# Performance work log

Hardware: AMD Instinct MI355X
Metric: run time of the kernel (lower is better)

## Reference

```python
import jax, jax.numpy as jnp
import numpy as np

HEADS = 4
ALPHA = 0.2
NEG = -9.0e15


def _layer(h, adj_mask, W, linW, linb, qkvW, qkvb, a, concat):
    # One GraphSelfAttentionLayer (eval mode: dropout off).
    F_out = W.shape[-1]
    n = h.shape[0]
    Wh = (h @ W) @ linW + linb                      # [N, F]
    qkv = Wh @ qkvW + qkvb                          # [N, 3F]
    q, k, v = jnp.split(qkv, 3, axis=-1)
    to_heads = lambda t: t.reshape(n, HEADS, F_out // HEADS).transpose(1, 0, 2)
    q, k, v = to_heads(q), to_heads(k), to_heads(v)  # [H, N, d]
    # note: scale uses out_features (not per-head d), matching the source
    dots = jax.nn.softmax(jnp.einsum('hid,hjd->hij', q, k) * (F_out ** -0.5), axis=-1)
    Wh0 = jnp.einsum('hij,hjd->hid', dots, v).transpose(1, 0, 2).reshape(n, F_out)
    Wh0 = jax.nn.softmax(Wh0, axis=-1)
    # decomposed all-pairs GAT score: e[i,j] = leakyrelu(Wh_i.a1 + Wh_j.a2)
    f1 = Wh @ a[:F_out]                             # [N]
    f2 = Wh @ a[F_out:]
    e = jax.nn.leaky_relu(f1[:, None] + f2[None, :], ALPHA)
    logits = jnp.where(adj_mask, e + dots.sum(0), NEG)
    att = jax.nn.softmax(logits, axis=1)
    hp = att @ Wh + Wh0
    return jax.nn.elu(hp) if concat else hp


def setup_inputs() -> dict:
    key = jax.random.key(0)
    ks = jax.random.split(key, 16)
    N, NFEAT, NHID, NOUT, H = 3072, 128, 32, 64, 4
    s = 0.1
    return {
        'x': jax.random.normal(ks[0], (N, NFEAT), jnp.float32),
        'adj': jax.random.randint(ks[1], (N, N), 0, 2, dtype=jnp.int32),
        'W_h': jax.random.normal(ks[2], (H, NFEAT, NHID), jnp.float32) * s,
        'lin_W_h': jax.random.normal(ks[3], (H, NHID, NHID), jnp.float32) * s,
        'lin_b_h': jax.random.normal(ks[4], (H, NHID), jnp.float32) * s,
        'qkv_W_h': jax.random.normal(ks[5], (H, NHID, 3 * NHID), jnp.float32) * s,
        'qkv_b_h': jax.random.normal(ks[6], (H, 3 * NHID), jnp.float32) * s,
        'a_h': jax.random.normal(ks[7], (H, 2 * NHID), jnp.float32) * s,
        'W_o': jax.random.normal(ks[8], (NHID * H, NOUT), jnp.float32) * s,
        'lin_W_o': jax.random.normal(ks[9], (NOUT, NOUT), jnp.float32) * s,
        'lin_b_o': jax.random.normal(ks[10], (NOUT,), jnp.float32) * s,
        'qkv_W_o': jax.random.normal(ks[11], (NOUT, 3 * NOUT), jnp.float32) * s,
        'qkv_b_o': jax.random.normal(ks[12], (3 * NOUT,), jnp.float32) * s,
        'a_o': jax.random.normal(ks[13], (2 * NOUT,), jnp.float32) * s,
    }


def reference(x, adj, W_h, lin_W_h, lin_b_h, qkv_W_h, qkv_b_h, a_h,
              W_o, lin_W_o, lin_b_o, qkv_W_o, qkv_b_o, a_o):
    mask = adj > 0
    heads_out = jax.vmap(
        lambda W, lW, lb, qW, qb, a: _layer(x, mask, W, lW, lb, qW, qb, a, True)
    )(W_h, lin_W_h, lin_b_h, qkv_W_h, qkv_b_h, a_h)      # [H, N, NHID]
    n = x.shape[0]
    x1 = jax.nn.elu(heads_out.transpose(1, 0, 2).reshape(n, -1))  # cat(dim=1) then elu
    out = jax.nn.elu(_layer(x1, mask, W_o, lin_W_o, lin_b_o, qkv_W_o, qkv_b_o, a_o, False))
    return out
```

## Files before the change

### kernel.cpp

```cpp
#include <hip/hip_runtime.h>
#include <hip/hip_bf16.h>

#define LOG2E 1.4426950408889634f
#define LOG2LOG2E 0.5287663729448977f

typedef unsigned int u32;
typedef float f32x16 __attribute__((ext_vector_type(16)));
typedef short sh8 __attribute__((ext_vector_type(8)));

union FR { u32 u[4]; sh8 s; };

__device__ __forceinline__ u32 cvt_pk_bf16(float lo, float hi){
  u32 r;
  asm volatile("v_cvt_pk_bf16_f32 %0, %1, %2" : "=v"(r) : "v"(lo), "v"(hi));
  return r;
}

__device__ __forceinline__ float asum16(const float* s){
  float a0=s[0]+s[8],  a1=s[1]+s[9],  a2=s[2]+s[10], a3=s[3]+s[11];
  float a4=s[4]+s[12], a5=s[5]+s[13], a6=s[6]+s[14], a7=s[7]+s[15];
  a0+=a4; a1+=a5; a2+=a6; a3+=a7;
  a0+=a2; a1+=a3;
  return a0+a1;
}

template<int W>
__device__ __forceinline__ float wred_max(float v){
  #pragma unroll
  for (int o=1;o<W;o<<=1) v = fmaxf(v, __shfl_xor(v,o));
  return v;
}
template<int W>
__device__ __forceinline__ float wred_sum(float v){
  #pragma unroll
  for (int o=1;o<W;o<<=1) v += __shfl_xor(v,o);
  return v;
}

__global__ __launch_bounds__(256) void k_mask(const int* __restrict__ adj, u32* __restrict__ mk){
  int id = blockIdx.x*256 + threadIdx.x;
  const int4* src = (const int4*)(adj + (size_t)id*32);
  u32 m = 0;
  #pragma unroll
  for (int g=0; g<8; g++){
    int4 v = src[g];
    if (v.x>0) m |= 1u<<(g*4+0);
    if (v.y>0) m |= 1u<<(g*4+1);
    if (v.z>0) m |= 1u<<(g*4+2);
    if (v.w>0) m |= 1u<<(g*4+3);
  }
  mk[id] = m;
}

template<int FIN, int F>
__global__ __launch_bounds__(256) void k_pre_a(const float* __restrict__ xg, const float* __restrict__ Wg,
    const float* __restrict__ lWg, const float* __restrict__ lbg, float* __restrict__ Whg, int N)
{
  const int h = blockIdx.y;
  const int row = blockIdx.x*256 + threadIdx.x;
  __shared__ float Wl[FIN*F];
  __shared__ float lWl[F*F];
  __shared__ float lbl[F];
  for (int i=threadIdx.x;i<FIN*F;i+=256) Wl[i]=Wg[(size_t)h*FIN*F+i];
  for (int i=threadIdx.x;i<F*F;i+=256) lWl[i]=lWg[(size_t)h*F*F+i];
  if (threadIdx.x<F) lbl[threadIdx.x]=lbg[h*F+threadIdx.x];
  __syncthreads();
  float t[F];
  #pragma unroll
  for (int c=0;c<F;c++) t[c]=0.f;
  const float4* xr = (const float4*)(xg + (size_t)row*FIN);
  for (int k4=0;k4<FIN/4;k4++){
    float4 xv = xr[k4];
    float xs[4]={xv.x,xv.y,xv.z,xv.w};
    #pragma unroll
    for (int kk=0;kk<4;kk++){
      float x1 = xs[kk];
      const float* wrow = Wl + (k4*4+kk)*F;
      #pragma unroll
      for (int c=0;c<F;c++) t[c] = fmaf(x1, wrow[c], t[c]);
    }
  }
  float wh[F];
  #pragma unroll
  for (int c=0;c<F;c++) wh[c]=lbl[c];
  #pragma unroll
  for (int k=0;k<F;k++){
    float tv=t[k];
    #pragma unroll
    for (int c=0;c<F;c++) wh[c]=fmaf(tv, lWl[k*F+c], wh[c]);
  }
  float4* dst=(float4*)(Whg + ((size_t)h*N+row)*F);
  #pragma unroll
  for (int c4=0;c4<F/4;c4++) dst[c4]=make_float4(wh[c4*4],wh[c4*4+1],wh[c4*4+2],wh[c4*4+3]);
}

template<int F, int GPR>
__global__ __launch_bounds__(256) void k_pre_b(const float* __restrict__ Whg, const float* __restrict__ qWg,
   const float* __restrict__ qbg, const float* __restrict__ ag,
   float* __restrict__ qg, float* __restrict__ kg, float* __restrict__ vg,
   float* __restrict__ f1g, float* __restrict__ f2g, int N)
{
  constexpr int ROWS = 256/GPR;
  constexpr int GC3  = 3*F/GPR;
  const int h = blockIdx.y;
  const int rl = threadIdx.x / GPR, grp = threadIdx.x % GPR;
  const int row = blockIdx.x*ROWS + rl;
  __shared__ float qWl[F*3*F];
  __shared__ float qbl[3*F];
  __shared__ float al[2*F];
  __shared__ float whl[ROWS][F+1];
  for (int i=threadIdx.x;i<F*3*F;i+=256) qWl[i]=qWg[(size_t)h*F*3*F+i];
  if (threadIdx.x<3*F) qbl[threadIdx.x]=qbg[h*3*F+threadIdx.x];
  if (threadIdx.x<2*F) al[threadIdx.x]=ag[h*2*F+threadIdx.x];
  {
    const float4* wsrc = (const float4*)(Whg + ((size_t)h*N+row)*F);
    #pragma unroll
    for (int c4=0;c4<2;c4++){
      float4 t = wsrc[grp*2+c4];
      int b = grp*8+c4*4;
      whl[rl][b]=t.x; whl[rl][b+1]=t.y; whl[rl][b+2]=t.z; whl[rl][b+3]=t.w;
    }
  }
  __syncthreads();
  float acc[GC3];
  #pragma unroll
  for (int c=0;c<GC3;c++) acc[c]=qbl[grp*GC3+c];
  for (int k=0;k<F;k++){
    float wv = whl[rl][k];
    #pragma unroll
    for (int c=0;c<GC3;c++) acc[c]=fmaf(wv, qWl[k*3*F + grp*GC3 + c], acc[c]);
  }
  size_t base = ((size_t)h*N+row)*F;
  #pragma unroll
  for (int c=0;c<GC3;c++){
    int col = grp*GC3+c;
    if (col < F)        qg[base+col]       = acc[c];
    else if (col < 2*F) kg[base+col-F]     = acc[c];
    else                vg[base+col-2*F]   = acc[c];
  }
  if (grp<2){
    const float* av = al + grp*F;
    float s=0.f;
    for (int k=0;k<F;k++) s = fmaf(whl[rl][k], av[k], s);
    (grp? f2g:f1g)[(size_t)h*N+row] = s;
  }
}

template<int S>
__global__ __launch_bounds__(256,4) void k_sweep1_mfma32(const float* __restrict__ qg, const float* __restrict__ kg,
    const float* __restrict__ vg, float* __restrict__ pml, float* __restrict__ pw, int N, float qscale)
{
  constexpr int F=32, LROW=33;
  const int h = blockIdx.z;
  const int sc = blockIdx.y;
  const int JC = N/S;
  const int wid = threadIdx.x>>6;
  const int lane = threadIdx.x&63;
  const int l31 = lane&31;
  const int half = lane>>5;
  const int itile = blockIdx.x*4 + wid;
  const int i = itile*32 + l31;
  __shared__ float vt[32*LROW];

  sh8 qf[4];
  {
    const float* qrow = qg + ((size_t)h*N + i)*F;
    #pragma unroll
    for (int hh=0;hh<4;hh++){
      FR u;
      #pragma unroll
      for (int p=0;p<4;p++){
        float lo = half? 0.f : qrow[hh*8+2*p]*qscale;
        float hi = half? 0.f : qrow[hh*8+2*p+1]*qscale;
        u.u[p] = cvt_pk_bf16(lo,hi);
      }
      qf[hh]=u.s;
    }
  }
  f32x16 C, Zv;
  #pragma unroll
  for (int r=0;r<16;r++){ C[r]=0.f; Zv[r]=0.f; }
  float l[4];
  #pragma unroll
  for (int hh=0;hh<4;hh++) l[hh]=0.f;
  const sh8 zf = {0,0,0,0,0,0,0,0};

  const int j0 = sc*JC;
  for (int jt=0; jt<JC; jt+=32){
    __syncthreads();
    {
      const float4* vs = (const float4*)(vg + ((size_t)h*N + j0+jt)*F);
      int idx = threadIdx.x;
      int j = idx>>3, c4 = idx&7;
      float4 b = vs[idx];
      float* vd = vt + j*LROW + c4*4;
      vd[0]=b.x; vd[1]=b.y; vd[2]=b.z; vd[3]=b.w;
    }
    __syncthreads();
    const float* krow = kg + ((size_t)h*N + j0+jt + l31)*F;
    sh8 vA[2];
    #pragma unroll
    for (int c=0;c<2;c++){
      FR u;
      #pragma unroll
      for (int p=0;p<4;p++){
        int jl = c*16 + half*8 + 2*p;
        u.u[p]=cvt_pk_bf16(vt[jl*LROW + l31], vt[(jl+1)*LROW + l31]);
      }
      vA[c]=u.s;
    }
    #pragma unroll
    for (int hh=0;hh<4;hh++){
      sh8 kf;
      {
        FR u;
        float4 ka = *(const float4*)(krow + hh*8);
        float4 kb = *(const float4*)(krow + hh*8 + 4);
        u.u[0]=cvt_pk_bf16(ka.x,ka.y);
        u.u[1]=cvt_pk_bf16(ka.z,ka.w);
        u.u[2]=cvt_pk_bf16(kb.x,kb.y);
        u.u[3]=cvt_pk_bf16(kb.z,kb.w);
        kf=u.s;
      }
      f32x16 Sacc = __builtin_amdgcn_mfma_f32_32x32x16_bf16(kf, qf[hh], Zv, 0,0,0);
      float p[16];
      #pragma unroll
      for (int r=0;r<16;r++) p[r] = exp2f(Sacc[r]);
      l[hh] += asum16(p);
      const bool own = ((l31>>3)==hh);
      #pragma unroll
      for (int c=0;c<2;c++){
        u32 a01 = cvt_pk_bf16(p[c*8+0], p[c*8+1]);
        u32 a23 = cvt_pk_bf16(p[c*8+2], p[c*8+3]);
        u32 b01 = cvt_pk_bf16(p[c*8+4], p[c*8+5]);
        u32 b23 = cvt_pk_bf16(p[c*8+6], p[c*8+7]);
        u32 a01s = __shfl_xor(a01,32);
        u32 a23s = __shfl_xor(a23,32);
        u32 b01s = __shfl_xor(b01,32);
        u32 b23s = __shfl_xor(b23,32);
        FR bf;
        bf.u[0] = half? b01s : a01;
        bf.u[1] = half? b23s : a23;
        bf.u[2] = half? b01  : a01s;
        bf.u[3] = half? b23  : a23s;
        sh8 av = own ? vA[c] : zf;
        C = __builtin_amdgcn_mfma_f32_32x32x16_bf16(av, bf.s, C, 0,0,0);
      }
    }
  }
  float lt[4];
  #pragma unroll
  for (int hh=0;hh<4;hh++) lt[hh] = l[hh] + __shfl_xor(l[hh],32);
  if (half==0){
    float* pb = pml + ((size_t)(h*S+sc)*8)*N + i;
    #pragma unroll
    for (int hh=0;hh<4;hh++){ pb[(size_t)hh*N]=0.f; pb[(size_t)(4+hh)*N]=lt[hh]; }
  }
  {
    float* pv = pw + ((size_t)(h*S+sc)*N + i)*F;
    #pragma unroll
    for (int hh=0;hh<4;hh++){
      *(float4*)(pv + 8*hh + 4*half) = make_float4(C[hh*4],C[hh*4+1],C[hh*4+2],C[hh*4+3]);
    }
  }
}

template<int S>
__global__ __launch_bounds__(256,4) void k_sweep2_mfma32(const float* __restrict__ qg, const float* __restrict__ kg,
    const float* __restrict__ whg, const float* __restrict__ f1g, const float* __restrict__ f2g,
    const float* __restrict__ mstar, const float* __restrict__ invl, const u32* __restrict__ mk,
    float* __restrict__ p2ml, float* __restrict__ php, int N, float qscale)
{
  constexpr int F=32, LROW=33;
  const int h = blockIdx.z;
  const int sc = blockIdx.y;
  const int JC = N/S;
  const int wid = threadIdx.x>>6;
  const int lane = threadIdx.x&63;
  const int l31 = lane&31;
  const int half = lane>>5;
  const int itile = blockIdx.x*4 + wid;
  const int i = itile*32 + l31;
  const int nw = N>>5;
  __shared__ float wt[32*LROW];
  __shared__ float f2s[32];

  sh8 qf[4];
  {
    const float* qrow = qg + ((size_t)h*N + i)*F;
    #pragma unroll
    for (int hh=0;hh<4;hh++){
      FR u;
      #pragma unroll
      for (int p=0;p<4;p++){
        float lo = half? 0.f : qrow[hh*8+2*p]*qscale;
        float hi = half? 0.f : qrow[hh*8+2*p+1]*qscale;
        u.u[p] = cvt_pk_bf16(lo,hi);
      }
      qf[hh]=u.s;
    }
  }
  float cc[4];
  #pragma unroll
  for (int hh=0;hh<4;hh++){
    float msv = mstar[((size_t)(h*4+hh))*N+i];
    float ilv = invl [((size_t)(h*4+hh))*N+i];
    cc[hh] = log2f(ilv) - msv + LOG2LOG2E;
  }
  const float f1 = f1g[(size_t)h*N+i];
  f32x16 C, Zv;
  #pragma unroll
  for (int r=0;r<16;r++){ C[r]=0.f; Zv[r]=0.f; }
  float L=0.f;

  const int j0 = sc*JC;
  for (int jt=0; jt<JC; jt+=32){
    __syncthreads();
    {
      const float4* ws = (const float4*)(whg + ((size_t)h*N + j0+jt)*F);
      int idx = threadIdx.x;
      int j = idx>>3, c4 = idx&7;
      float4 b = ws[idx];
      float* wd = wt + j*LROW + c4*4;
      wd[0]=b.x; wd[1]=b.y; wd[2]=b.z; wd[3]=b.w;
      if (threadIdx.x<32) f2s[threadIdx.x] = f2g[(size_t)h*N + j0+jt+threadIdx.x];
    }
    __syncthreads();
    const float* krow = kg + ((size_t)h*N + j0+jt + l31)*F;
    float ds[16];
    #pragma unroll
    for (int r=0;r<16;r++) ds[r]=0.f;
    #pragma unroll
    for (int hh=0;hh<4;hh++){
      sh8 kf;
      {
        FR u;
        float4 ka = *(const float4*)(krow + hh*8);
        float4 kb = *(const float4*)(krow + hh*8 + 4);
        u.u[0]=cvt_pk_bf16(ka.x,ka.y);
        u.u[1]=cvt_pk_bf16(ka.z,ka.w);
        u.u[2]=cvt_pk_bf16(kb.x,kb.y);
        u.u[3]=cvt_pk_bf16(kb.z,kb.w);
        kf=u.s;
      }
      f32x16 Sacc = __builtin_amdgcn_mfma_f32_32x32x16_bf16(kf, qf[hh], Zv, 0,0,0);
      float ch = cc[hh];
      #pragma unroll
      for (int r=0;r<16;r++) ds[r] += exp2f(Sacc[r] + ch);
    }
    u32 mw = mk[(size_t)i*nw + ((j0+jt)>>5)];
    float w[16];
    #pragma unroll
    for (int r=0;r<16;r++){
      int jo = (r&3)+8*(r>>2)+4*half;
      float e = f1 + f2s[jo];
      e = (e>=0.f)? e : 0.2f*e;
      float ev = exp2f(fmaf(e, LOG2E, ds[r]));
      w[r] = ((mw>>jo)&1u) ? ev : 0.f;
    }
    L += asum16(w);
    #pragma unroll
    for (int c=0;c<2;c++){
      sh8 whA;
      {
        FR u;
        #pragma unroll
        for (int p=0;p<4;p++){
          int jl = c*16 + half*8 + 2*p;
          u.u[p]=cvt_pk_bf16(wt[jl*LROW + l31], wt[(jl+1)*LROW + l31]);
        }
        whA=u.s;
      }
      u32 a01 = cvt_pk_bf16(w[c*8+0], w[c*8+1]);
      u32 a23 = cvt_pk_bf16(w[c*8+2], w[c*8+3]);
      u32 b01 = cvt_pk_bf16(w[c*8+4], w[c*8+5]);
      u32 b23 = cvt_pk_bf16(w[c*8+6], w[c*8+7]);
      u32 a01s = __shfl_xor(a01,32);
      u32 a23s = __shfl_xor(a23,32);
      u32 b01s = __shfl_xor(b01,32);
      u32 b23s = __shfl_xor(b23,32);
      FR bf;
      bf.u[0] = half? b01s : a01;
      bf.u[1] = half? b23s : a23;
      bf.u[2] = half? b01  : a01s;
      bf.u[3] = half? b23  : a23s;
      C = __builtin_amdgcn_mfma_f32_32x32x16_bf16(whA, bf.s, C, 0,0,0);
    }
  }
  L = L + __shfl_xor(L,32);
  if (half==0){
    float* pb = p2ml + ((size_t)(h*S+sc)*2)*N + i;
    pb[0]=0.f; pb[(size_t)N]=L;
  }
  {
    float* pv = php + ((size_t)(h*S+sc)*N + i)*F;
    #pragma unroll
    for (int g=0;g<4;g++)
      *(float4*)(pv + 8*g + 4*half) = make_float4(C[g*4],C[g*4+1],C[g*4+2],C[g*4+3]);
  }
}

template<int S>
__global__ __launch_bounds__(256,4) void k_sweep1_mfma64(const float* __restrict__ qg, const float* __restrict__ kg,
    const float* __restrict__ vg, float* __restrict__ pml, float* __restrict__ pw, int N, float qscale)
{
  constexpr int F=64, LROW=65;
  const int h = blockIdx.z;
  const int sc = blockIdx.y;
  const int JC = N/S;
  const int wid = threadIdx.x>>6;
  const int lane = threadIdx.x&63;
  const int l31 = lane&31;
  const int half = lane>>5;
  const int itile = blockIdx.x*4 + wid;
  const int i = itile*32 + l31;
  __shared__ float vt[32*LROW];

  sh8 qf[4];
  {
    const float* qrow = qg + ((size_t)h*N + i)*F;
    #pragma unroll
    for (int hh=0;hh<4;hh++){
      FR u;
      #pragma unroll
      for (int p=0;p<4;p++)
        u.u[p] = cvt_pk_bf16(qrow[hh*16 + 8*half + 2*p]*qscale, qrow[hh*16 + 8*half + 2*p+1]*qscale);
      qf[hh]=u.s;
    }
  }
  f32x16 C0, C1, Zv;
  #pragma unroll
  for (int r=0;r<16;r++){ C0[r]=0.f; C1[r]=0.f; Zv[r]=0.f; }
  float l[4];
  #pragma unroll
  for (int hh=0;hh<4;hh++) l[hh]=0.f;
  const sh8 zf = {0,0,0,0,0,0,0,0};

  const int j0 = sc*JC;
  for (int jt=0; jt<JC; jt+=32){
    __syncthreads();
    {
      const float4* vs = (const float4*)(vg + ((size_t)h*N + j0+jt)*F);
      #pragma unroll
      for (int q2=0;q2<2;q2++){
        int idx = q2*256 + threadIdx.x;
        int j = idx>>4, c4 = idx&15;
        float4 b = vs[idx];
        float* vd = vt + j*LROW + c4*4;
        vd[0]=b.x; vd[1]=b.y; vd[2]=b.z; vd[3]=b.w;
      }
    }
    __syncthreads();
    const float* krow = kg + ((size_t)h*N + j0+jt + l31)*F;
    sh8 vA[2][2];
    #pragma unroll
    for (int ch=0;ch<2;ch++)
      #pragma unroll
      for (int c=0;c<2;c++){
        FR u;
        #pragma unroll
        for (int p=0;p<4;p++){
          int jl = c*16 + half*8 + 2*p;
          u.u[p]=cvt_pk_bf16(vt[jl*LROW + ch*32 + l31], vt[(jl+1)*LROW + ch*32 + l31]);
        }
        vA[ch][c]=u.s;
      }
    #pragma unroll
    for (int hh=0;hh<4;hh++){
      sh8 kf;
      {
        FR u;
        float4 ka = *(const float4*)(krow + hh*16 + 8*half);
        float4 kb = *(const float4*)(krow + hh*16 + 8*half + 4);
        u.u[0]=cvt_pk_bf16(ka.x,ka.y);
        u.u[1]=cvt_pk_bf16(ka.z,ka.w);
        u.u[2]=cvt_pk_bf16(kb.x,kb.y);
        u.u[3]=cvt_pk_bf16(kb.z,kb.w);
        kf=u.s;
      }
      f32x16 Sacc = __builtin_amdgcn_mfma_f32_32x32x16_bf16(kf, qf[hh], Zv, 0,0,0);
      f32x16 &Cr = (hh>>1)? C1 : C0;
      float p[16];
      #pragma unroll
      for (int r=0;r<16;r++) p[r] = exp2f(Sacc[r]);
      l[hh] += asum16(p);
      const bool own = ((l31>>4) == (hh&1));
      #pragma unroll
      for (int c=0;c<2;c++){
        u32 a01 = cvt_pk_bf16(p[c*8+0], p[c*8+1]);
        u32 a23 = cvt_pk_bf16(p[c*8+2], p[c*8+3]);
        u32 b01 = cvt_pk_bf16(p[c*8+4], p[c*8+5]);
        u32 b23 = cvt_pk_bf16(p[c*8+6], p[c*8+7]);
        u32 a01s = __shfl_xor(a01,32);
        u32 a23s = __shfl_xor(a23,32);
        u32 b01s = __shfl_xor(b01,32);
        u32 b23s = __shfl_xor(b23,32);
        FR bf;
        bf.u[0] = half? b01s : a01;
        bf.u[1] = half? b23s : a23;
        bf.u[2] = half? b01  : a01s;
        bf.u[3] = half? b23  : a23s;
        sh8 av = own ? vA[hh>>1][c] : zf;
        Cr = __builtin_amdgcn_mfma_f32_32x32x16_bf16(av, bf.s, Cr, 0,0,0);
      }
    }
  }
  float lt[4];
  #pragma unroll
  for (int hh=0;hh<4;hh++) lt[hh] = l[hh] + __shfl_xor(l[hh],32);
  if (half==0){
    float* pb = pml + ((size_t)(h*S+sc)*8)*N + i;
    #pragma unroll
    for (int hh=0;hh<4;hh++){ pb[(size_t)hh*N]=0.f; pb[(size_t)(4+hh)*N]=lt[hh]; }
  }
  {
    float* pv = pw + ((size_t)(h*S+sc)*N + i)*F;
    #pragma unroll
    for (int g=0;g<4;g++){
      *(float4*)(pv + 8*g + 4*half)      = make_float4(C0[g*4],C0[g*4+1],C0[g*4+2],C0[g*4+3]);
      *(float4*)(pv + 32 + 8*g + 4*half) = make_float4(C1[g*4],C1[g*4+1],C1[g*4+2],C1[g*4+3]);
    }
  }
}

template<int S>
__global__ __launch_bounds__(256,4) void k_sweep2_mfma64(const float* __restrict__ qg, const float* __restrict__ kg,
    const float* __restrict__ whg, const float* __restrict__ f1g, const float* __restrict__ f2g,
    const float* __restrict__ mstar, const float* __restrict__ invl, const u32* __restrict__ mk,
    float* __restrict__ p2ml, float* __restrict__ php, int N, float qscale)
{
  constexpr int F=64, LROW=65;
  const int h = blockIdx.z;
  const int sc = blockIdx.y;
  const int JC = N/S;
  const int wid = threadIdx.x>>6;
  const int lane = threadIdx.x&63;
  const int l31 = lane&31;
  const int half = lane>>5;
  const int itile = blockIdx.x*4 + wid;
  const int i = itile*32 + l31;
  const int nw = N>>5;
  __shared__ float wt[32*LROW];
  __shared__ float f2s[32];

  sh8 qf[4];
  {
    const float* qrow = qg + ((size_t)h*N + i)*F;
    #pragma unroll
    for (int hh=0;hh<4;hh++){
      FR u;
      #pragma unroll
      for (int p=0;p<4;p++)
        u.u[p] = cvt_pk_bf16(qrow[hh*16 + 8*half + 2*p]*qscale, qrow[hh*16 + 8*half + 2*p+1]*qscale);
      qf[hh]=u.s;
    }
  }
  float cc[4];
  #pragma unroll
  for (int hh=0;hh<4;hh++){
    float msv = mstar[((size_t)(h*4+hh))*N+i];
    float ilv = invl [((size_t)(h*4+hh))*N+i];
    cc[hh] = log2f(ilv) - msv + LOG2LOG2E;
  }
  const float f1 = f1g[(size_t)h*N+i];
  f32x16 C0, C1, Zv;
  #pragma unroll
  for (int r=0;r<16;r++){ C0[r]=0.f; C1[r]=0.f; Zv[r]=0.f; }
  float L=0.f;

  const int j0 = sc*JC;
  for (int jt=0; jt<JC; jt+=32){
    __syncthreads();
    {
      const float4* ws = (const float4*)(whg + ((size_t)h*N + j0+jt)*F);
      #pragma unroll
      for (int q2=0;q2<2;q2++){
        int idx = q2*256 + threadIdx.x;
        int j = idx>>4, c4 = idx&15;
        float4 b = ws[idx];
        float* wd = wt + j*LROW + c4*4;
        wd[0]=b.x; wd[1]=b.y; wd[2]=b.z; wd[3]=b.w;
      }
      if (threadIdx.x<32) f2s[threadIdx.x] = f2g[(size_t)h*N + j0+jt+threadIdx.x];
    }
    __syncthreads();
    const float* krow = kg + ((size_t)h*N + j0+jt + l31)*F;
    float ds[16];
    #pragma unroll
    for (int r=0;r<16;r++) ds[r]=0.f;
    #pragma unroll
    for (int hh=0;hh<4;hh++){
      sh8 kf;
      {
        FR u;
        float4 ka = *(const float4*)(krow + hh*16 + 8*half);
        float4 kb = *(const float4*)(krow + hh*16 + 8*half + 4);
        u.u[0]=cvt_pk_bf16(ka.x,ka.y);
        u.u[1]=cvt_pk_bf16(ka.z,ka.w);
        u.u[2]=cvt_pk_bf16(kb.x,kb.y);
        u.u[3]=cvt_pk_bf16(kb.z,kb.w);
        kf=u.s;
      }
      f32x16 Sacc = __builtin_amdgcn_mfma_f32_32x32x16_bf16(kf, qf[hh], Zv, 0,0,0);
      float ch = cc[hh];
      #pragma unroll
      for (int r=0;r<16;r++) ds[r] += exp2f(Sacc[r] + ch);
    }
    u32 mw = mk[(size_t)i*nw + ((j0+jt)>>5)];
    float w[16];
    #pragma unroll
    for (int r=0;r<16;r++){
      int jo = (r&3)+8*(r>>2)+4*half;
      float e = f1 + f2s[jo];
      e = (e>=0.f)? e : 0.2f*e;
      float ev = exp2f(fmaf(e, LOG2E, ds[r]));
      w[r] = ((mw>>jo)&1u) ? ev : 0.f;
    }
    L += asum16(w);
    #pragma unroll
    for (int c=0;c<2;c++){
      u32 a01 = cvt_pk_bf16(w[c*8+0], w[c*8+1]);
      u32 a23 = cvt_pk_bf16(w[c*8+2], w[c*8+3]);
      u32 b01 = cvt_pk_bf16(w[c*8+4], w[c*8+5]);
      u32 b23 = cvt_pk_bf16(w[c*8+6], w[c*8+7]);
      u32 a01s = __shfl_xor(a01,32);
      u32 a23s = __shfl_xor(a23,32);
      u32 b01s = __shfl_xor(b01,32);
      u32 b23s = __shfl_xor(b23,32);
      FR bf;
      bf.u[0] = half? b01s : a01;
      bf.u[1] = half? b23s : a23;
      bf.u[2] = half? b01  : a01s;
      bf.u[3] = half? b23  : a23s;
      #pragma unroll
      for (int ch=0;ch<2;ch++){
        sh8 whA;
        {
          FR u;
          #pragma unroll
          for (int p=0;p<4;p++){
            int jl = c*16 + half*8 + 2*p;
            u.u[p]=cvt_pk_bf16(wt[jl*LROW + ch*32 + l31], wt[(jl+1)*LROW + ch*32 + l31]);
          }
          whA=u.s;
        }
        if (ch) C1 = __builtin_amdgcn_mfma_f32_32x32x16_bf16(whA, bf.s, C1, 0,0,0);
        else    C0 = __builtin_amdgcn_mfma_f32_32x32x16_bf16(whA, bf.s, C0, 0,0,0);
      }
    }
  }
  L = L + __shfl_xor(L,32);
  if (half==0){
    float* pb = p2ml + ((size_t)(h*S+sc)*2)*N + i;
    pb[0]=0.f; pb[(size_t)N]=L;
  }
  {
    float* pv = php + ((size_t)(h*S+sc)*N + i)*F;
    #pragma unroll
    for (int g=0;g<4;g++){
      *(float4*)(pv + 8*g + 4*half)      = make_float4(C0[g*4],C0[g*4+1],C0[g*4+2],C0[g*4+3]);
      *(float4*)(pv + 32 + 8*g + 4*half) = make_float4(C1[g*4],C1[g*4+1],C1[g*4+2],C1[g*4+3]);
    }
  }
}

template<int S>
__global__ __launch_bounds__(256) void k_stats1(const float* __restrict__ pml, float* __restrict__ wgt1,
    float* __restrict__ mstar, float* __restrict__ invl, int N)
{
  const int h = blockIdx.y>>2, hh = blockIdx.y&3;
  const int row = blockIdx.x*256 + threadIdx.x;
  float mv[S];
  #pragma unroll
  for (int sc=0;sc<S;sc++) mv[sc]=pml[((size_t)((h*S+sc)*8)+hh)*N+row];
  float ms=-1e30f;
  #pragma unroll
  for (int sc=0;sc<S;sc++) ms=fmaxf(ms,mv[sc]);
  float ls=0.f;
  #pragma unroll
  for (int sc=0;sc<S;sc++){
    float w = exp2f(mv[sc]-ms);
    float lv = pml[((size_t)((h*S+sc)*8)+4+hh)*N+row];
    ls = fmaf(lv, w, ls);
    wgt1[((size_t)((h*S+sc)*4)+hh)*N+row]=w;
  }
  mstar[((size_t)(h*4+hh))*N+row]=ms;
  invl [((size_t)(h*4+hh))*N+row]=1.f/ls;
}

template<int F, int S>
__global__ __launch_bounds__(256) void k_comb1(const float* __restrict__ pw, const float* __restrict__ wgt1,
    const float* __restrict__ invl, float* __restrict__ smw, int N)
{
  constexpr int D = F/4;
  constexpr int RPB = 256/F;
  const int h = blockIdx.y;
  const int c = threadIdx.x % F;
  const int row = blockIdx.x*RPB + threadIdx.x / F;
  const int hh = c / D;
  float acc=0.f;
  #pragma unroll
  for (int sc=0;sc<S;sc++){
    float w = wgt1[((size_t)((h*S+sc)*4)+hh)*N+row];
    float p = pw[((size_t)(h*S+sc)*N + row)*F + c];
    acc = fmaf(w,p,acc);
  }
  float w0 = acc * invl[((size_t)(h*4+hh))*N+row];
  float mx = wred_max<F>(w0);
  float e = exp2f((w0-mx)*LOG2E);
  float sm = wred_sum<F>(e);
  smw[((size_t)h*N+row)*F + c] = e/sm;
}

template<int S>
__global__ __launch_bounds__(256) void k_stats2(const float* __restrict__ p2ml, float* __restrict__ wgt2,
    float* __restrict__ invL, int N)
{
  const int h = blockIdx.y;
  const int row = blockIdx.x*256 + threadIdx.x;
  float mv[S];
  #pragma unroll
  for (int sc=0;sc<S;sc++) mv[sc]=p2ml[((size_t)((h*S+sc)*2))*N+row];
  float M=-1e30f;
  #pragma unroll
  for (int sc=0;sc<S;sc++) M=fmaxf(M,mv[sc]);
  float L=0.f;
  #pragma unroll
  for (int sc=0;sc<S;sc++){
    float w=exp2f(mv[sc]-M);
    float lv=p2ml[((size_t)((h*S+sc)*2)+1)*N+row];
    L = fmaf(lv,w,L);
    wgt2[(size_t)(h*S+sc)*N+row]=w;
  }
  invL[(size_t)h*N+row]=1.f/L;
}

template<int F, int S, bool L1OUT>
__global__ __launch_bounds__(256) void k_comb2(const float* __restrict__ php, const float* __restrict__ wgt2,
    const float* __restrict__ invL, const float* __restrict__ smw, void* __restrict__ outp, int N)
{
  constexpr int RPB = 256/F;
  const int h = blockIdx.y;
  const int c = threadIdx.x % F;
  const int row = blockIdx.x*RPB + threadIdx.x / F;
  float acc=0.f;
  #pragma unroll
  for (int sc=0;sc<S;sc++){
    float w = wgt2[(size_t)(h*S+sc)*N+row];
    float p = php[((size_t)(h*S+sc)*N + row)*F + c];
    acc = fmaf(w,p,acc);
  }
  float v = acc * invL[(size_t)h*N+row] + smw[((size_t)h*N+row)*F + c];
  v = (v>0.f)? v : expm1f(v);
  if (L1OUT){
    v = (v>0.f)? v : expm1f(v);
    ((float*)outp)[(size_t)row*(4*F) + h*F + c] = v;
  } else {
    ((float*)outp)[(size_t)row*F + c] = v;
  }
}

extern "C" void kernel_launch(void* const* d_in, const int* in_sizes, int n_in,
                              void* d_out, int out_size, void* d_ws, size_t ws_size,
                              hipStream_t stream)
{
  (void)in_sizes; (void)n_in; (void)out_size; (void)ws_size;
  const int N=3072;
  const int S1=8, S2=32;

  const float* x      = (const float*)d_in[0];
  const int*   adj    = (const int*)d_in[1];
  const float* W_h    = (const float*)d_in[2];
  const float* linW_h = (const float*)d_in[3];
  const float* linb_h = (const float*)d_in[4];
  const float* qkvW_h = (const float*)d_in[5];
  const float* qkvb_h = (const float*)d_in[6];
  const float* a_h    = (const float*)d_in[7];
  const float* W_o    = (const float*)d_in[8];
  const float* linW_o = (const float*)d_in[9];
  const float* linb_o = (const float*)d_in[10];
  const float* qkvW_o = (const float*)d_in[11];
  const float* qkvb_o = (const float*)d_in[12];
  const float* a_o    = (const float*)d_in[13];

  char* w = (char*)d_ws;
  auto alloc=[&](size_t bytes)->char*{ char* p=w; w += (bytes+255)&~(size_t)255; return p; };
  u32*   mk    = (u32*)  alloc((size_t)N*(N/32)*4);
  float* Wh1   = (float*)alloc((size_t)4*N*32*4);
  float* q1    = (float*)alloc((size_t)4*N*32*4);
  float* k1    = (float*)alloc((size_t)4*N*32*4);
  float* v1    = (float*)alloc((size_t)4*N*32*4);
  float* f11   = (float*)alloc((size_t)4*N*4);
  float* f21   = (float*)alloc((size_t)4*N*4);
  float* smw1  = (float*)alloc((size_t)4*32*N*4);
  float* x1    = (float*)alloc((size_t)N*128*4);
  float* Wh2   = (float*)alloc((size_t)N*64*4);
  float* q2    = (float*)alloc((size_t)N*64*4);
  float* k2    = (float*)alloc((size_t)N*64*4);
  float* v2    = (float*)alloc((size_t)N*64*4);
  float* f12   = (float*)alloc((size_t)N*4);
  float* f22   = (float*)alloc((size_t)N*4);
  float* smw2  = (float*)alloc((size_t)64*N*4);
  float* mst   = (float*)alloc((size_t)16*N*4);
  float* ivl   = (float*)alloc((size_t)16*N*4);
  float* wgt1  = (float*)alloc((size_t)256*N*4);
  float* wgt2  = (float*)alloc((size_t)64*N*4);
  float* ivL   = (float*)alloc((size_t)4*N*4);
  float* pml   = (float*)alloc((size_t)512*N*4);
  float* pw    = (float*)alloc((size_t)2048*N*4);

  const float qs1 = 0.17677669529663687f * LOG2E;
  const float qs2 = 0.125f * LOG2E;

  k_mask<<<dim3(N*(N/32)/256), 256, 0, stream>>>(adj, mk);

  k_pre_a<128,32><<<dim3(N/256,4),256,0,stream>>>(x, W_h, linW_h, linb_h, Wh1, N);
  k_pre_b<32,4><<<dim3(N/64,4),256,0,stream>>>(Wh1, qkvW_h, qkvb_h, a_h, q1,k1,v1,f11,f21,N);
  k_sweep1_mfma32<8><<<dim3(N/128,S1,4),256,0,stream>>>(q1,k1,v1,pml,pw,N,qs1);
  k_stats1<8><<<dim3(N/256,16),256,0,stream>>>(pml,wgt1,mst,ivl,N);
  k_comb1<32,8><<<dim3(N/8,4),256,0,stream>>>(pw,wgt1,ivl,smw1,N);
  k_sweep2_mfma32<8><<<dim3(N/128,S1,4),256,0,stream>>>(q1,k1,Wh1,f11,f21,mst,ivl,mk,pml,pw,N,qs1);
  k_stats2<8><<<dim3(N/256,4),256,0,stream>>>(pml,wgt2,ivL,N);
  k_comb2<32,8,true><<<dim3(N/8,4),256,0,stream>>>(pw,wgt2,ivL,smw1,x1,N);

  k_pre_a<128,64><<<dim3(N/256,1),256,0,stream>>>(x1, W_o, linW_o, linb_o, Wh2, N);
  k_pre_b<64,8><<<dim3(N/32,1),256,0,stream>>>(Wh2, qkvW_o, qkvb_o, a_o, q2,k2,v2,f12,f22,N);
  k_sweep1_mfma64<32><<<dim3(N/128,S2,1),256,0,stream>>>(q2,k2,v2,pml,pw,N,qs2);
  k_stats1<32><<<dim3(N/256,4),256,0,stream>>>(pml,wgt1,mst,ivl,N);
  k_comb1<64,32><<<dim3(N/4,1),256,0,stream>>>(pw,wgt1,ivl,smw2,N);
  k_sweep2_mfma64<32><<<dim3(N/128,S2,1),256,0,stream>>>(q2,k2,Wh2,f12,f22,mst,ivl,mk,pml,pw,N,qs2);
  k_stats2<32><<<dim3(N/256,1),256,0,stream>>>(pml,wgt2,ivL,N);
  k_comb2<64,32,false><<<dim3(N/4,1),256,0,stream>>>(pw,wgt2,ivL,smw2,d_out,N);
}
```

Measured before the change: 380.6 us.

## Store V, Wh and mask transposed so sweeps load operands directly without LDS staging

Producers now write V, Wh and the packed adjacency mask in transposed layouts (feature-major, word-major), so the sweep kernels read MFMA A-operands with contiguous float4 global loads instead of staging tiles through shared memory with two barriers per iteration. The leaky-relu edge term is also computed before the score MFMAs, reading f2 directly from global memory. This removes the LDS round trip and block-wide syncs in the inner loop. In exchange, pre_a/pre_b/mask perform strided, uncoalesced transposed writes, and more global traffic now relies on caching.

```diff
diff --git a/kernel.cpp b/kernel.cpp
--- a/kernel.cpp
+++ b/kernel.cpp
@@ -37,9 +37,11 @@
   return v;
 }
 
-__global__ __launch_bounds__(256) void k_mask(const int* __restrict__ adj, u32* __restrict__ mk){
+template<int NW>
+__global__ __launch_bounds__(256) void k_mask(const int* __restrict__ adj, u32* __restrict__ mkT, int N){
   int id = blockIdx.x*256 + threadIdx.x;
-  const int4* src = (const int4*)(adj + (size_t)id*32);
+  int row = id / NW, word = id - row*NW;
+  const int4* src = (const int4*)(adj + (size_t)row*N + word*32);
   u32 m = 0;
   #pragma unroll
   for (int g=0; g<8; g++){
@@ -49,12 +51,13 @@
     if (v.z>0) m |= 1u<<(g*4+2);
     if (v.w>0) m |= 1u<<(g*4+3);
   }
-  mk[id] = m;
+  mkT[(size_t)word*N + row] = m;
 }
 
 template<int FIN, int F>
 __global__ __launch_bounds__(256) void k_pre_a(const float* __restrict__ xg, const float* __restrict__ Wg,
-    const float* __restrict__ lWg, const float* __restrict__ lbg, float* __restrict__ Whg, int N)
+    const float* __restrict__ lWg, const float* __restrict__ lbg,
+    float* __restrict__ Whg, float* __restrict__ WhTg, int N)
 {
   const int h = blockIdx.y;
   const int row = blockIdx.x*256 + threadIdx.x;
@@ -92,12 +95,14 @@
   float4* dst=(float4*)(Whg + ((size_t)h*N+row)*F);
   #pragma unroll
   for (int c4=0;c4<F/4;c4++) dst[c4]=make_float4(wh[c4*4],wh[c4*4+1],wh[c4*4+2],wh[c4*4+3]);
+  #pragma unroll
+  for (int c=0;c<F;c++) WhTg[((size_t)(h*F+c))*N + row] = wh[c];
 }
 
 template<int F, int GPR>
 __global__ __launch_bounds__(256) void k_pre_b(const float* __restrict__ Whg, const float* __restrict__ qWg,
    const float* __restrict__ qbg, const float* __restrict__ ag,
-   float* __restrict__ qg, float* __restrict__ kg, float* __restrict__ vg,
+   float* __restrict__ qg, float* __restrict__ kg, float* __restrict__ vTg,
    float* __restrict__ f1g, float* __restrict__ f2g, int N)
 {
   constexpr int ROWS = 256/GPR;
@@ -136,7 +141,7 @@
     int col = grp*GC3+c;
     if (col < F)        qg[base+col]       = acc[c];
     else if (col < 2*F) kg[base+col-F]     = acc[c];
-    else                vg[base+col-2*F]   = acc[c];
+    else                vTg[((size_t)(h*F + col-2*F))*N + row] = acc[c];
   }
   if (grp<2){
     const float* av = al + grp*F;
@@ -148,9 +153,9 @@
 
 template<int S>
 __global__ __launch_bounds__(256,4) void k_sweep1_mfma32(const float* __restrict__ qg, const float* __restrict__ kg,
-    const float* __restrict__ vg, float* __restrict__ pml, float* __restrict__ pw, int N, float qscale)
-{
-  constexpr int F=32, LROW=33;
+    const float* __restrict__ vTg, float* __restrict__ pml, float* __restrict__ pw, int N, float qscale)
+{
+  constexpr int F=32;
   const int h = blockIdx.z;
   const int sc = blockIdx.y;
   const int JC = N/S;
@@ -160,7 +165,6 @@
   const int half = lane>>5;
   const int itile = blockIdx.x*4 + wid;
   const int i = itile*32 + l31;
-  __shared__ float vt[32*LROW];
 
   sh8 qf[4];
   {
@@ -186,27 +190,21 @@
   const sh8 zf = {0,0,0,0,0,0,0,0};
 
   const int j0 = sc*JC;
+  const float* vTrow = vTg + ((size_t)(h*F + l31))*N + j0;
+  const float* kbase = kg + ((size_t)h*N + j0 + l31)*F;
   for (int jt=0; jt<JC; jt+=32){
-    __syncthreads();
-    {
-      const float4* vs = (const float4*)(vg + ((size_t)h*N + j0+jt)*F);
-      int idx = threadIdx.x;
-      int j = idx>>3, c4 = idx&7;
-      float4 b = vs[idx];
-      float* vd = vt + j*LROW + c4*4;
-      vd[0]=b.x; vd[1]=b.y; vd[2]=b.z; vd[3]=b.w;
-    }
-    __syncthreads();
-    const float* krow = kg + ((size_t)h*N + j0+jt + l31)*F;
+    const float* krow = kbase + (size_t)jt*F;
     sh8 vA[2];
     #pragma unroll
     for (int c=0;c<2;c++){
+      const float* vp = vTrow + jt + c*16 + half*8;
+      float4 va = *(const float4*)vp;
+      float4 vb = *(const float4*)(vp+4);
       FR u;
-      #pragma unroll
-      for (int p=0;p<4;p++){
-        int jl = c*16 + half*8 + 2*p;
-        u.u[p]=cvt_pk_bf16(vt[jl*LROW + l31], vt[(jl+1)*LROW + l31]);
-      }
+      u.u[0]=cvt_pk_bf16(va.x,va.y);
+      u.u[1]=cvt_pk_bf16(va.z,va.w);
+      u.u[2]=cvt_pk_bf16(vb.x,vb.y);
+      u.u[3]=cvt_pk_bf16(vb.z,vb.w);
       vA[c]=u.s;
     }
     #pragma unroll
@@ -267,11 +265,11 @@
 
 template<int S>
 __global__ __launch_bounds__(256,4) void k_sweep2_mfma32(const float* __restrict__ qg, const float* __restrict__ kg,
-    const float* __restrict__ whg, const float* __restrict__ f1g, const float* __restrict__ f2g,
-    const float* __restrict__ mstar, const float* __restrict__ invl, const u32* __restrict__ mk,
+    const float* __restrict__ whTg, const float* __restrict__ f1g, const float* __restrict__ f2g,
+    const float* __restrict__ mstar, const float* __restrict__ invl, const u32* __restrict__ mkT,
     float* __restrict__ p2ml, float* __restrict__ php, int N, float qscale)
 {
-  constexpr int F=32, LROW=33;
+  constexpr int F=32;
   const int h = blockIdx.z;
   const int sc = blockIdx.y;
   const int JC = N/S;
@@ -281,9 +279,6 @@
   const int half = lane>>5;
   const int itile = blockIdx.x*4 + wid;
   const int i = itile*32 + l31;
-  const int nw = N>>5;
-  __shared__ float wt[32*LROW];
-  __shared__ float f2s[32];
 
   sh8 qf[4];
   {
@@ -314,19 +309,19 @@
   float L=0.f;
 
   const int j0 = sc*JC;
+  const float* whTrow = whTg + ((size_t)(h*F + l31))*N + j0;
+  const float* kbase = kg + ((size_t)h*N + j0 + l31)*F;
+  const float* f2b = f2g + (size_t)h*N + j0;
   for (int jt=0; jt<JC; jt+=32){
-    __syncthreads();
-    {
-      const float4* ws = (const float4*)(whg + ((size_t)h*N + j0+jt)*F);
-      int idx = threadIdx.x;
-      int j = idx>>3, c4 = idx&7;
-      float4 b = ws[idx];
-      float* wd = wt + j*LROW + c4*4;
-      wd[0]=b.x; wd[1]=b.y; wd[2]=b.z; wd[3]=b.w;
-      if (threadIdx.x<32) f2s[threadIdx.x] = f2g[(size_t)h*N + j0+jt+threadIdx.x];
-    }
-    __syncthreads();
-    const float* krow = kg + ((size_t)h*N + j0+jt + l31)*F;
+    u32 mw = mkT[(size_t)((j0+jt)>>5)*N + i];
+    const float* krow = kbase + (size_t)jt*F;
+    float ew[16];
+    #pragma unroll
+    for (int r=0;r<16;r++){
+      int jo = (r&3)+8*(r>>2)+4*half;
+      float e = f1 + f2b[jt+jo];
+      ew[r] = (e>=0.f)? e : 0.2f*e;
+    }
     float ds[16];
     #pragma unroll
     for (int r=0;r<16;r++) ds[r]=0.f;
@@ -348,33 +343,31 @@
       #pragma unroll
       for (int r=0;r<16;r++) ds[r] += exp2f(Sacc[r] + ch);
     }
-    u32 mw = mk[(size_t)i*nw + ((j0+jt)>>5)];
-    float w[16];
     #pragma unroll
     for (int r=0;r<16;r++){
       int jo = (r&3)+8*(r>>2)+4*half;
-      float e = f1 + f2s[jo];
-      e = (e>=0.f)? e : 0.2f*e;
-      float ev = exp2f(fmaf(e, LOG2E, ds[r]));
-      w[r] = ((mw>>jo)&1u) ? ev : 0.f;
-    }
-    L += asum16(w);
+      float ev = exp2f(fmaf(ew[r], LOG2E, ds[r]));
+      ds[r] = ((mw>>jo)&1u) ? ev : 0.f;
+    }
+    L += asum16(ds);
     #pragma unroll
     for (int c=0;c<2;c++){
       sh8 whA;
       {
+        const float* wp = whTrow + jt + c*16 + half*8;
+        float4 wa = *(const float4*)wp;
+        float4 wb = *(const float4*)(wp+4);
         FR u;
-        #pragma unroll
-        for (int p=0;p<4;p++){
-          int jl = c*16 + half*8 + 2*p;
-          u.u[p]=cvt_pk_bf16(wt[jl*LROW + l31], wt[(jl+1)*LROW + l31]);
-        }
+        u.u[0]=cvt_pk_bf16(wa.x,wa.y);
+        u.u[1]=cvt_pk_bf16(wa.z,wa.w);
+        u.u[2]=cvt_pk_bf16(wb.x,wb.y);
+        u.u[3]=cvt_pk_bf16(wb.z,wb.w);
         whA=u.s;
       }
-      u32 a01 = cvt_pk_bf16(w[c*8+0], w[c*8+1]);
-      u32 a23 = cvt_pk_bf16(w[c*8+2], w[c*8+3]);
-      u32 b01 = cvt_pk_bf16(w[c*8+4], w[c*8+5]);
-      u32 b23 = cvt_pk_bf16(w[c*8+6], w[c*8+7]);
+      u32 a01 = cvt_pk_bf16(ds[c*8+0], ds[c*8+1]);
+      u32 a23 = cvt_pk_bf16(ds[c*8+2], ds[c*8+3]);
+      u32 b01 = cvt_pk_bf16(ds[c*8+4], ds[c*8+5]);
+      u32 b23 = cvt_pk_bf16(ds[c*8+6], ds[c*8+7]);
       u32 a01s = __shfl_xor(a01,32);
       u32 a23s = __shfl_xor(a23,32);
       u32 b01s = __shfl_xor(b01,32);
@@ -402,9 +395,9 @@
 
 template<int S>
 __global__ __launch_bounds__(256,4) void k_sweep1_mfma64(const float* __restrict__ qg, const float* __restrict__ kg,
-    const float* __restrict__ vg, float* __restrict__ pml, float* __restrict__ pw, int N, float qscale)
-{
-  constexpr int F=64, LROW=65;
+    const float* __restrict__ vTg, float* __restrict__ pml, float* __restrict__ pw, int N, float qscale)
+{
+  constexpr int F=64;
   const int h = blockIdx.z;
   const int sc = blockIdx.y;
   const int JC = N/S;
@@ -414,7 +407,6 @@
   const int half = lane>>5;
   const int itile = blockIdx.x*4 + wid;
   const int i = itile*32 + l31;
-  __shared__ float vt[32*LROW];
 
   sh8 qf[4];
   {
@@ -437,34 +429,28 @@
   const sh8 zf = {0,0,0,0,0,0,0,0};
 
   const int j0 = sc*JC;
+  const float* vTrow0 = vTg + ((size_t)(h*F + l31))*N + j0;
+  const float* vTrow1 = vTg + ((size_t)(h*F + 32 + l31))*N + j0;
+  const float* kbase = kg + ((size_t)h*N + j0 + l31)*F;
   for (int jt=0; jt<JC; jt+=32){
-    __syncthreads();
-    {
-      const float4* vs = (const float4*)(vg + ((size_t)h*N + j0+jt)*F);
-      #pragma unroll
-      for (int q2=0;q2<2;q2++){
-        int idx = q2*256 + threadIdx.x;
-        int j = idx>>4, c4 = idx&15;
-        float4 b = vs[idx];
-        float* vd = vt + j*LROW + c4*4;
-        vd[0]=b.x; vd[1]=b.y; vd[2]=b.z; vd[3]=b.w;
-      }
-    }
-    __syncthreads();
-    const float* krow = kg + ((size_t)h*N + j0+jt + l31)*F;
+    const float* krow = kbase + (size_t)jt*F;
     sh8 vA[2][2];
     #pragma unroll
-    for (int ch=0;ch<2;ch++)
+    for (int ch=0;ch<2;ch++){
+      const float* vr = ch? vTrow1 : vTrow0;
       #pragma unroll
       for (int c=0;c<2;c++){
+        const float* vp = vr + jt + c*16 + half*8;
+        float4 va = *(const float4*)vp;
+        float4 vb = *(const float4*)(vp+4);
         FR u;
-        #pragma unroll
-        for (int p=0;p<4;p++){
-          int jl = c*16 + half*8 + 2*p;
-          u.u[p]=cvt_pk_bf16(vt[jl*LROW + ch*32 + l31], vt[(jl+1)*LROW + ch*32 + l31]);
-        }
+        u.u[0]=cvt_pk_bf16(va.x,va.y);
+        u.u[1]=cvt_pk_bf16(va.z,va.w);
+        u.u[2]=cvt_pk_bf16(vb.x,vb.y);
+        u.u[3]=cvt_pk_bf16(vb.z,vb.w);
         vA[ch][c]=u.s;
       }
+    }
     #pragma unroll
     for (int hh=0;hh<4;hh++){
       sh8 kf;
@@ -525,11 +511,11 @@
 
 template<int S>
 __global__ __launch_bounds__(256,4) void k_sweep2_mfma64(const float* __restrict__ qg, const float* __restrict__ kg,
-    const float* __restrict__ whg, const float* __restrict__ f1g, const float* __restrict__ f2g,
-    const float* __restrict__ mstar, const float* __restrict__ invl, const u32* __restrict__ mk,
+    const float* __restrict__ whTg, const float* __restrict__ f1g, const float* __restrict__ f2g,
+    const float* __restrict__ mstar, const float* __restrict__ invl, const u32* __restrict__ mkT,
     float* __restrict__ p2ml, float* __restrict__ php, int N, float qscale)
 {
-  constexpr int F=64, LROW=65;
+  constexpr int F=64;
   const int h = blockIdx.z;
   const int sc = blockIdx.y;
   const int JC = N/S;
@@ -539,9 +525,6 @@
   const int half = lane>>5;
   const int itile = blockIdx.x*4 + wid;
   const int i = itile*32 + l31;
-  const int nw = N>>5;
-  __shared__ float wt[32*LROW];
-  __shared__ float f2s[32];
 
   sh8 qf[4];
   {
@@ -569,22 +552,20 @@
   float L=0.f;
 
   const int j0 = sc*JC;
+  const float* whTrow0 = whTg + ((size_t)(h*F + l31))*N + j0;
+  const float* whTrow1 = whTg + ((size_t)(h*F + 32 + l31))*N + j0;
+  const float* kbase = kg + ((size_t)h*N + j0 + l31)*F;
+  const float* f2b = f2g + (size_t)h*N + j0;
   for (int jt=0; jt<JC; jt+=32){
-    __syncthreads();
-    {
-      const float4* ws = (const float4*)(whg + ((size_t)h*N + j0+jt)*F);
-      #pragma unroll
-      for (int q2=0;q2<2;q2++){
-        int idx = q2*256 + threadIdx.x;
-        int j = idx>>4, c4 = idx&15;
-        float4 b = ws[idx];
-        float* wd = wt + j*LROW + c4*4;
-        wd[0]=b.x; wd[1]=b.y; wd[2]=b.z; wd[3]=b.w;
-      }
-      if (threadIdx.x<32) f2s[threadIdx.x] = f2g[(size_t)h*N + j0+jt+threadIdx.x];
-    }
-    __syncthreads();
-    const float* krow = kg + ((size_t)h*N + j0+jt + l31)*F;
+    u32 mw = mkT[(size_t)((j0+jt)>>5)*N + i];
+    const float* krow = kbase + (size_t)jt*F;
+    float ew[16];
+    #pragma unroll
+    for (int r=0;r<16;r++){
+      int jo = (r&3)+8*(r>>2)+4*half;
+      float e = f1 + f2b[jt+jo];
+      ew[r] = (e>=0.f)? e : 0.2f*e;
+    }
     float ds[16];
     #pragma unroll
     for (int r=0;r<16;r++) ds[r]=0.f;
@@ -606,23 +587,19 @@
       #pragma unroll
       for (int r=0;r<16;r++) ds[r] += exp2f(Sacc[r] + ch);
     }
-    u32 mw = mk[(size_t)i*nw + ((j0+jt)>>5)];
-    float w[16];
     #pragma unroll
     for (int r=0;r<16;r++){
       int jo = (r&3)+8*(r>>2)+4*half;
-      float e = f1 + f2s[jo];
-      e = (e>=0.f)? e : 0.2f*e;
-      float ev = exp2f(fmaf(e, LOG2E, ds[r]));
-      w[r] = ((mw>>jo)&1u) ? ev : 0.f;
-    }
-    L += asum16(w);
+      float ev = exp2f(fmaf(ew[r], LOG2E, ds[r]));
+      ds[r] = ((mw>>jo)&1u) ? ev : 0.f;
+    }
+    L += asum16(ds);
     #pragma unroll
     for (int c=0;c<2;c++){
-      u32 a01 = cvt_pk_bf16(w[c*8+0], w[c*8+1]);
-      u32 a23 = cvt_pk_bf16(w[c*8+2], w[c*8+3]);
-      u32 b01 = cvt_pk_bf16(w[c*8+4], w[c*8+5]);
-      u32 b23 = cvt_pk_bf16(w[c*8+6], w[c*8+7]);
+      u32 a01 = cvt_pk_bf16(ds[c*8+0], ds[c*8+1]);
+      u32 a23 = cvt_pk_bf16(ds[c*8+2], ds[c*8+3]);
+      u32 b01 = cvt_pk_bf16(ds[c*8+4], ds[c*8+5]);
+      u32 b23 = cvt_pk_bf16(ds[c*8+6], ds[c*8+7]);
       u32 a01s = __shfl_xor(a01,32);
       u32 a23s = __shfl_xor(a23,32);
       u32 b01s = __shfl_xor(b01,32);
@@ -636,12 +613,14 @@
       for (int ch=0;ch<2;ch++){
         sh8 whA;
         {
+          const float* wp = (ch? whTrow1 : whTrow0) + jt + c*16 + half*8;
+          float4 wa = *(const float4*)wp;
+          float4 wb = *(const float4*)(wp+4);
           FR u;
-          #pragma unroll
-          for (int p=0;p<4;p++){
-            int jl = c*16 + half*8 + 2*p;
-            u.u[p]=cvt_pk_bf16(wt[jl*LROW + ch*32 + l31], wt[(jl+1)*LROW + ch*32 + l31]);
-          }
+          u.u[0]=cvt_pk_bf16(wa.x,wa.y);
+          u.u[1]=cvt_pk_bf16(wa.z,wa.w);
+          u.u[2]=cvt_pk_bf16(wb.x,wb.y);
+          u.u[3]=cvt_pk_bf16(wb.z,wb.w);
           whA=u.s;
         }
         if (ch) C1 = __builtin_amdgcn_mfma_f32_32x32x16_bf16(whA, bf.s, C1, 0,0,0);
@@ -785,19 +764,21 @@
 
   char* w = (char*)d_ws;
   auto alloc=[&](size_t bytes)->char*{ char* p=w; w += (bytes+255)&~(size_t)255; return p; };
-  u32*   mk    = (u32*)  alloc((size_t)N*(N/32)*4);
+  u32*   mkT   = (u32*)  alloc((size_t)N*(N/32)*4);
   float* Wh1   = (float*)alloc((size_t)4*N*32*4);
+  float* Wh1T  = (float*)alloc((size_t)4*N*32*4);
   float* q1    = (float*)alloc((size_t)4*N*32*4);
   float* k1    = (float*)alloc((size_t)4*N*32*4);
-  float* v1    = (float*)alloc((size_t)4*N*32*4);
+  float* v1T   = (float*)alloc((size_t)4*N*32*4);
   float* f11   = (float*)alloc((size_t)4*N*4);
   float* f21   = (float*)alloc((size_t)4*N*4);
   float* smw1  = (float*)alloc((size_t)4*32*N*4);
   float* x1    = (float*)alloc((size_t)N*128*4);
   float* Wh2   = (float*)alloc((size_t)N*64*4);
+  float* Wh2T  = (float*)alloc((size_t)N*64*4);
   float* q2    = (float*)alloc((size_t)N*64*4);
   float* k2    = (float*)alloc((size_t)N*64*4);
-  float* v2    = (float*)alloc((size_t)N*64*4);
+  float* v2T   = (float*)alloc((size_t)N*64*4);
   float* f12   = (float*)alloc((size_t)N*4);
   float* f22   = (float*)alloc((size_t)N*4);
   float* smw2  = (float*)alloc((size_t)64*N*4);
@@ -812,23 +793,23 @@
   const float qs1 = 0.17677669529663687f * LOG2E;
   const float qs2 = 0.125f * LOG2E;
 
-  k_mask<<<dim3(N*(N/32)/256), 256, 0, stream>>>(adj, mk);
-
-  k_pre_a<128,32><<<dim3(N/256,4),256,0,stream>>>(x, W_h, linW_h, linb_h, Wh1, N);
-  k_pre_b<32,4><<<dim3(N/64,4),256,0,stream>>>(Wh1, qkvW_h, qkvb_h, a_h, q1,k1,v1,f11,f21,N);
-  k_sweep1_mfma32<8><<<dim3(N/128,S1,4),256,0,stream>>>(q1,k1,v1,pml,pw,N,qs1);
+  k_mask<96><<<dim3(N*(N/32)/256), 256, 0, stream>>>(adj, mkT, N);
+
+  k_pre_a<128,32><<<dim3(N/256,4),256,0,stream>>>(x, W_h, linW_h, linb_h, Wh1, Wh1T, N);
+  k_pre_b<32,4><<<dim3(N/64,4),256,0,stream>>>(Wh1, qkvW_h, qkvb_h, a_h, q1,k1,v1T,f11,f21,N);
+  k_sweep1_mfma32<8><<<dim3(N/128,S1,4),256,0,stream>>>(q1,k1,v1T,pml,pw,N,qs1);
   k_stats1<8><<<dim3(N/256,16),256,0,stream>>>(pml,wgt1,mst,ivl,N);
   k_comb1<32,8><<<dim3(N/8,4),256,0,stream>>>(pw,wgt1,ivl,smw1,N);
-  k_sweep2_mfma32<8><<<dim3(N/128,S1,4),256,0,stream>>>(q1,k1,Wh1,f11,f21,mst,ivl,mk,pml,pw,N,qs1);
+  k_sweep2_mfma32<8><<<dim3(N/128,S1,4),256,0,stream>>>(q1,k1,Wh1T,f11,f21,mst,ivl,mkT,pml,pw,N,qs1);
   k_stats2<8><<<dim3(N/256,4),256,0,stream>>>(pml,wgt2,ivL,N);
   k_comb2<32,8,true><<<dim3(N/8,4),256,0,stream>>>(pw,wgt2,ivL,smw1,x1,N);
 
-  k_pre_a<128,64><<<dim3(N/256,1),256,0,stream>>>(x1, W_o, linW_o, linb_o, Wh2, N);
-  k_pre_b<64,8><<<dim3(N/32,1),256,0,stream>>>(Wh2, qkvW_o, qkvb_o, a_o, q2,k2,v2,f12,f22,N);
-  k_sweep1_mfma64<32><<<dim3(N/128,S2,1),256,0,stream>>>(q2,k2,v2,pml,pw,N,qs2);
+  k_pre_a<128,64><<<dim3(N/256,1),256,0,stream>>>(x1, W_o, linW_o, linb_o, Wh2, Wh2T, N);
+  k_pre_b<64,8><<<dim3(N/32,1),256,0,stream>>>(Wh2, qkvW_o, qkvb_o, a_o, q2,k2,v2T,f12,f22,N);
+  k_sweep1_mfma64<32><<<dim3(N/128,S2,1),256,0,stream>>>(q2,k2,v2T,pml,pw,N,qs2);
   k_stats1<32><<<dim3(N/256,4),256,0,stream>>>(pml,wgt1,mst,ivl,N);
   k_comb1<64,32><<<dim3(N/4,1),256,0,stream>>>(pw,wgt1,ivl,smw2,N);
-  k_sweep2_mfma64<32><<<dim3(N/128,S2,1),256,0,stream>>>(q2,k2,Wh2,f12,f22,mst,ivl,mk,pml,pw,N,qs2);
+  k_sweep2_mfma64<32><<<dim3(N/128,S2,1),256,0,stream>>>(q2,k2,Wh2T,f12,f22,mst,ivl,mkT,pml,pw,N,qs2);
   k_stats2<32><<<dim3(N/256,1),256,0,stream>>>(pml,wgt2,ivL,N);
   k_comb2<64,32,false><<<dim3(N/4,1),256,0,stream>>>(pw,wgt2,ivL,smw2,d_out,N);
 }
```

Result: slower. 402.7 us (+5.8%).
